# Performance work log

Hardware: AMD Instinct MI355X
Metric: run time of the kernel (lower is better)

## Reference

```python
import jax, jax.numpy as jnp
import numpy as np

N1, N2 = 262144, 65536          # dense / coarse point counts (packed batch)
PREV, SKIP, M0, M1 = 512, 256, 256, 256
EPS_BN = 1e-5                    # torch BatchNorm1d default eps
EPS_DIST = 1e-8


def _bn(x, g, b):
    # BatchNorm1d in training mode: biased batch stats over the point axis
    m = x.mean(axis=0)
    v = x.var(axis=0)
    return (x - m) * jax.lax.rsqrt(v + EPS_BN) * g + b


def setup_inputs() -> dict:
    key = jax.random.key(0)
    ks = jax.random.split(key, 8)
    inp = {
        "points1": jax.random.normal(ks[0], (N1, SKIP), jnp.float32),
        "points2": jax.random.normal(ks[1], (N2, PREV), jnp.float32),
        "dist": jax.random.uniform(ks[2], (N1, 3), jnp.float32),
        "idx": jax.random.randint(ks[3], (N1, 3), 0, N2, dtype=jnp.int32),
        # mlp_f0 / norm_f0
        "Wf0": jax.random.normal(ks[4], (PREV, M0), jnp.float32) / np.sqrt(PREV).astype(np.float32),
        "bf0": jnp.zeros((M0,), jnp.float32),
        "gf0": jnp.ones((M0,), jnp.float32),
        "betaf0": jnp.zeros((M0,), jnp.float32),
        # mlp_s0 / norm_s0 (skip path)
        "Ws0": jax.random.normal(ks[5], (SKIP, M0), jnp.float32) / np.sqrt(SKIP).astype(np.float32),
        "bs0": jnp.zeros((M0,), jnp.float32),
        "gs0": jnp.ones((M0,), jnp.float32),
        "betas0": jnp.zeros((M0,), jnp.float32),
        # mlp_convs[0] / mlp_bns[0]
        "W1": jax.random.normal(ks[6], (M0, M1), jnp.float32) / np.sqrt(M0).astype(np.float32),
        "b1": jnp.zeros((M1,), jnp.float32),
        "g1": jnp.ones((M1,), jnp.float32),
        "beta1": jnp.zeros((M1,), jnp.float32),
    }
    return inp


def reference(points1, points2, dist, idx, Wf0, bf0, gf0, betaf0,
              Ws0, bs0, gs0, betas0, W1, b1, g1, beta1):
    # f0 MLP + BN on coarse features: [N2, PREV] -> [N2, M0]
    p2 = _bn(points2 @ Wf0 + bf0, gf0, betaf0)
    # inverse-distance weights over 3 neighbors: [N1, 3]
    dr = 1.0 / (dist + EPS_DIST)
    w = dr / dr.sum(axis=1, keepdims=True)
    # fused gather + weighted sum: p2[idx] is [N1, 3, M0]
    interp = jnp.einsum('nkc,nk->nc', p2[idx], w)
    # skip path: [N1, SKIP] -> [N1, M0]
    skip = _bn(points1 @ Ws0 + bs0, gs0, betas0)
    x = jax.nn.relu(interp + skip)
    # mlp_convs stack (one layer here): Linear + BN + ReLU
    x = jax.nn.relu(_bn(x @ W1 + b1, g1, beta1))
    return x
```

## Files before the change

### kernel.cpp

```cpp
#include <hip/hip_runtime.h>
#include <hip/hip_bf16.h>

#define CN1 262144
#define CN2 65536
#define CPREV 512
#define CSKIP 256

using u16 = unsigned short;

typedef __attribute__((ext_vector_type(8))) short short8;
typedef __attribute__((ext_vector_type(8))) unsigned short ushort8;
typedef __attribute__((ext_vector_type(4))) float f32x4;
typedef __attribute__((ext_vector_type(8))) float f32x8;

__device__ __forceinline__ float toF(float v) { return v; }
__device__ __forceinline__ float toF(u16 u) { return __uint_as_float(((unsigned)u) << 16); }
__device__ __forceinline__ u16 f2bf(float f) {
    unsigned b = __float_as_uint(f);
    b += 0x7FFFu + ((b >> 16) & 1u);
    return (u16)(b >> 16);
}
__device__ __forceinline__ unsigned pack2(float lo, float hi) {
    return ((unsigned)f2bf(hi) << 16) | (unsigned)f2bf(lo);
}

__global__ __launch_bounds__(256) void transpose_all(
    const float* __restrict__ Wf0, const float* __restrict__ Ws0,
    const float* __restrict__ W1,
    u16* __restrict__ Wtf0, u16* __restrict__ Wts0, u16* __restrict__ Wt1)
{
    int b = blockIdx.x;
    const float* W; u16* Wt; int ksh, e;
    if (b < 512)      { W = Wf0; Wt = Wtf0; ksh = 9; e = b * 256 + threadIdx.x; }
    else if (b < 768) { W = Ws0; Wt = Wts0; ksh = 8; e = (b - 512) * 256 + threadIdx.x; }
    else              { W = W1;  Wt = Wt1;  ksh = 8; e = (b - 768) * 256 + threadIdx.x; }
    int K = 1 << ksh;
    int n = e >> ksh;
    int k = e & (K - 1);
    Wt[e] = f2bf(W[((size_t)k << 8) + n]);
}

template<typename OT>
__device__ __forceinline__ void epilogue(
    f32x4 (&acc)[4][4], u16* AsU, u16* BsU,
    const float* __restrict__ bias, OT* __restrict__ C,
    float* __restrict__ partial, int bm, int t)
{
    const int lane = t & 63;
    const int wid = t >> 6;
    const int wr = wid >> 1;
    const int wrow = wid >> 2;
    const int wcol = wid & 3;
    __syncthreads();
    float* cs  = (float*)AsU;
    float* cs2 = ((float*)AsU) + 512;
    const int r4 = (lane >> 4) * 4;
    const int cc = lane & 15;
    float bv[4];
#pragma unroll
    for (int ni = 0; ni < 4; ++ni) bv[ni] = bias[wcol * 64 + ni * 16 + cc];

#pragma unroll
    for (int ni = 0; ni < 4; ++ni) {
        int col = wcol * 64 + ni * 16 + cc;
        float s = 0.f, s2 = 0.f;
#pragma unroll
        for (int mi = 0; mi < 4; ++mi) {
#pragma unroll
            for (int j = 0; j < 4; ++j) {
                float val = acc[mi][ni][j] + bv[ni];
                s += val;
                s2 = fmaf(val, val, s2);
            }
        }
        s  += __shfl_xor(s, 16);  s  += __shfl_xor(s, 32);
        s2 += __shfl_xor(s2, 16); s2 += __shfl_xor(s2, 32);
        if (lane < 16) { cs[wrow * 256 + col] = s; cs2[wrow * 256 + col] = s2; }
    }

    if constexpr (sizeof(OT) == 2) {
        u16* patchw = BsU + wid * (16 * 72);
        const int trow = lane >> 2;
        const int c16 = (lane & 3) * 16;
#pragma unroll
        for (int mi = 0; mi < 4; ++mi) {
            __syncthreads();
#pragma unroll
            for (int ni = 0; ni < 4; ++ni)
#pragma unroll
                for (int j = 0; j < 4; ++j)
                    patchw[(r4 + j) * 72 + ni * 16 + cc] = f2bf(acc[mi][ni][j] + bv[ni]);
            __syncthreads();
            ushort8 u0 = *(const ushort8*)&patchw[trow * 72 + c16];
            ushort8 u1 = *(const ushort8*)&patchw[trow * 72 + c16 + 8];
            size_t r = (size_t)bm + wrow * 64 + mi * 16 + trow;
            size_t cb = (size_t)wcol * 64 + c16;
            *(ushort8*)((u16*)C + r * 256 + cb) = u0;
            *(ushort8*)((u16*)C + r * 256 + cb + 8) = u1;
        }
    } else {
        float* patchf = ((float*)BsU) + wid * (16 * 36);
        const int trow = lane >> 2;
        const int c8 = (lane & 3) * 8;
#pragma unroll
        for (int mi = 0; mi < 4; ++mi) {
#pragma unroll
            for (int np = 0; np < 2; ++np) {
                __syncthreads();
#pragma unroll
                for (int h = 0; h < 2; ++h) {
                    int ni = np * 2 + h;
#pragma unroll
                    for (int j = 0; j < 4; ++j)
                        patchf[(r4 + j) * 36 + h * 16 + cc] = acc[mi][ni][j] + bv[ni];
                }
                __syncthreads();
                float4 v0 = *(float4*)&patchf[trow * 36 + c8];
                float4 v1 = *(float4*)&patchf[trow * 36 + c8 + 4];
                size_t r = (size_t)bm + wrow * 64 + mi * 16 + trow;
                size_t cb = (size_t)wcol * 64 + np * 32 + c8;
                *(float4*)((float*)C + r * 256 + cb) = v0;
                *(float4*)((float*)C + r * 256 + cb + 4) = v1;
            }
        }
    }
    __syncthreads();
    if (t < 256) {
        partial[(size_t)blockIdx.x * 512 + t]       = cs[t] + cs[256 + t];
        partial[(size_t)blockIdx.x * 512 + 256 + t] = cs2[t] + cs2[256 + t];
    }
    (void)wr;
}

template<int K, typename OT>
__global__ __launch_bounds__(512) void gemm_mfma(
    const float* __restrict__ Af, const u16* __restrict__ Wt,
    const float* __restrict__ bias, OT* __restrict__ C,
    float* __restrict__ partial)
{
    __shared__ u16 As[128 * 40];
    __shared__ u16 Bs[256 * 40];
    const int t = threadIdx.x;
    const int bm = blockIdx.x * 128;
    const int lane = t & 63;
    const int wid = t >> 6;
    const int wrow = wid >> 2;
    const int wcol = wid & 3;

    const int arow = t >> 2;
    const int koff = (t & 3) * 8;

    f32x4 acc[4][4] = {};

    float4 ga0A, ga1A, ga0B, ga1B;
    ushort8 gb0A, gb1A, gb0B, gb1B;

    auto LOADA = [&](int k0) {
        const float* p = Af + (size_t)(bm + arow) * K + k0 + koff;
        ga0A = *(const float4*)p;
        ga1A = *(const float4*)(p + 4);
        const u16* q = Wt + (size_t)arow * K + k0 + koff;
        gb0A = *(const ushort8*)q;
        gb1A = *(const ushort8*)(q + (size_t)128 * K);
    };
    auto LOADB = [&](int k0) {
        const float* p = Af + (size_t)(bm + arow) * K + k0 + koff;
        ga0B = *(const float4*)p;
        ga1B = *(const float4*)(p + 4);
        const u16* q = Wt + (size_t)arow * K + k0 + koff;
        gb0B = *(const ushort8*)q;
        gb1B = *(const ushort8*)(q + (size_t)128 * K);
    };
    auto STAGE = [&](const float4& g0, const float4& g1,
                     const ushort8& b0, const ushort8& b1) {
        uint4 w;
        w.x = pack2(g0.x, g0.y);
        w.y = pack2(g0.z, g0.w);
        w.z = pack2(g1.x, g1.y);
        w.w = pack2(g1.z, g1.w);
        *(uint4*)&As[arow * 40 + koff] = w;
        *(ushort8*)&Bs[arow * 40 + koff] = b0;
        *(ushort8*)&Bs[(128 + arow) * 40 + koff] = b1;
    };
    auto MMA = [&]() {
        const int kq = (lane >> 4) * 8;
        const int rr = lane & 15;
        short8 af[4];
#pragma unroll
        for (int mi = 0; mi < 4; ++mi)
            af[mi] = *(const short8*)&As[(wrow * 64 + mi * 16 + rr) * 40 + kq];
#pragma unroll
        for (int ni = 0; ni < 4; ++ni) {
            short8 bf = *(const short8*)&Bs[(wcol * 64 + ni * 16 + rr) * 40 + kq];
#pragma unroll
            for (int mi = 0; mi < 4; ++mi)
                acc[mi][ni] = __builtin_amdgcn_mfma_f32_16x16x32_bf16(
                    af[mi], bf, acc[mi][ni], 0, 0, 0);
        }
    };

    constexpr int nk = K >> 5;
    LOADA(0);
    LOADB(32);
#pragma unroll
    for (int it = 0; it < nk; it += 2) {
        __syncthreads();
        STAGE(ga0A, ga1A, gb0A, gb1A);
        __syncthreads();
        if (it + 2 < nk) LOADA((it + 2) << 5);
        MMA();
        __syncthreads();
        STAGE(ga0B, ga1B, gb0B, gb1B);
        __syncthreads();
        if (it + 3 < nk) LOADB((it + 3) << 5);
        MMA();
    }

    epilogue<OT>(acc, As, Bs, bias, C, partial, bm, t);
}

template<typename OT>
__global__ __launch_bounds__(512) void gemm_fused(
    const u16* __restrict__ skipb, const u16* __restrict__ y2,
    const float* __restrict__ dist, const int* __restrict__ idx,
    const float* __restrict__ ssf, const float* __restrict__ sss,
    const u16* __restrict__ Wt, const float* __restrict__ bias,
    OT* __restrict__ C, float* __restrict__ partial)
{
    constexpr int K = 256;
    __shared__ u16 As[128 * 40];
    __shared__ u16 Bs[256 * 40];
    __shared__ float sstab[768];
    const int t = threadIdx.x;
    const int bm = blockIdx.x * 128;
    const int lane = t & 63;
    const int wid = t >> 6;
    const int wrow = wid >> 2;
    const int wcol = wid & 3;

    const int arow = t >> 2;
    const int koff = (t & 3) * 8;
    const int row = bm + arow;

    for (int e = t; e < 768; e += 512)
        sstab[e] = (e < 256) ? ssf[e] : sss[e - 256];

    float d0 = dist[row * 3 + 0], d1 = dist[row * 3 + 1], d2 = dist[row * 3 + 2];
    float r0 = 1.f / (d0 + 1e-8f), r1 = 1.f / (d1 + 1e-8f), r2 = 1.f / (d2 + 1e-8f);
    float inv = 1.f / (r0 + r1 + r2);
    const float w0 = r0 * inv, w1 = r1 * inv, w2 = r2 * inv;
    const size_t i0 = (size_t)idx[row * 3 + 0];
    const size_t i1 = (size_t)idx[row * 3 + 1];
    const size_t i2 = (size_t)idx[row * 3 + 2];

    f32x4 acc[4][4] = {};

    ushort8 skA, a0A, a1A, a2A, gb0A, gb1A;
    ushort8 skB, a0B, a1B, a2B, gb0B, gb1B;

    auto LOADA = [&](int k0) {
        const int kc = k0 + koff;
        skA = *(const ushort8*)(skipb + (size_t)row * 256 + kc);
        a0A = *(const ushort8*)(y2 + i0 * 256 + kc);
        a1A = *(const ushort8*)(y2 + i1 * 256 + kc);
        a2A = *(const ushort8*)(y2 + i2 * 256 + kc);
        const u16* q = Wt + (size_t)arow * K + kc;
        gb0A = *(const ushort8*)q;
        gb1A = *(const ushort8*)(q + (size_t)128 * K);
    };
    auto LOADB = [&](int k0) {
        const int kc = k0 + koff;
        skB = *(const ushort8*)(skipb + (size_t)row * 256 + kc);
        a0B = *(const ushort8*)(y2 + i0 * 256 + kc);
        a1B = *(const ushort8*)(y2 + i1 * 256 + kc);
        a2B = *(const ushort8*)(y2 + i2 * 256 + kc);
        const u16* q = Wt + (size_t)arow * K + kc;
        gb0B = *(const ushort8*)q;
        gb1B = *(const ushort8*)(q + (size_t)128 * K);
    };
    auto STAGE = [&](int it, const ushort8& sk8, const ushort8& a0,
                     const ushort8& a1, const ushort8& a2,
                     const ushort8& b0, const ushort8& b1) {
        const int kc = (it << 5) + koff;
        f32x8 sf = *(const f32x8*)&sstab[kc];
        f32x8 sx = *(const f32x8*)&sstab[256 + kc];
        f32x8 ch = *(const f32x8*)&sstab[512 + kc];
        float xs[8];
#pragma unroll
        for (int j = 0; j < 8; ++j) {
            float iv = w0 * toF((u16)a0[j]) + w1 * toF((u16)a1[j])
                     + w2 * toF((u16)a2[j]);
            float val = fmaf(iv, sf[j], fmaf(toF((u16)sk8[j]), sx[j], ch[j]));
            xs[j] = fmaxf(val, 0.f);
        }
        uint4 w;
        w.x = pack2(xs[0], xs[1]);
        w.y = pack2(xs[2], xs[3]);
        w.z = pack2(xs[4], xs[5]);
        w.w = pack2(xs[6], xs[7]);
        *(uint4*)&As[arow * 40 + koff] = w;
        *(ushort8*)&Bs[arow * 40 + koff] = b0;
        *(ushort8*)&Bs[(128 + arow) * 40 + koff] = b1;
    };
    auto MMA = [&]() {
        const int kq = (lane >> 4) * 8;
        const int rr = lane & 15;
        short8 af[4];
#pragma unroll
        for (int mi = 0; mi < 4; ++mi)
            af[mi] = *(const short8*)&As[(wrow * 64 + mi * 16 + rr) * 40 + kq];
#pragma unroll
        for (int ni = 0; ni < 4; ++ni) {
            short8 bf = *(const short8*)&Bs[(wcol * 64 + ni * 16 + rr) * 40 + kq];
#pragma unroll
            for (int mi = 0; mi < 4; ++mi)
                acc[mi][ni] = __builtin_amdgcn_mfma_f32_16x16x32_bf16(
                    af[mi], bf, acc[mi][ni], 0, 0, 0);
        }
    };

    constexpr int nk = K >> 5;
    LOADA(0);
    LOADB(32);
#pragma unroll
    for (int it = 0; it < nk; it += 2) {
        __syncthreads();
        STAGE(it, skA, a0A, a1A, a2A, gb0A, gb1A);
        __syncthreads();
        if (it + 2 < nk) LOADA((it + 2) << 5);
        MMA();
        __syncthreads();
        STAGE(it + 1, skB, a0B, a1B, a2B, gb0B, gb1B);
        __syncthreads();
        if (it + 3 < nk) LOADB((it + 3) << 5);
        MMA();
    }

    epilogue<OT>(acc, As, Bs, bias, C, partial, bm, t);
}

__global__ __launch_bounds__(256) void colstats_final_par(
    const float* __restrict__ partial, int nb, float invR,
    const float* __restrict__ g, const float* __restrict__ beta,
    const float* __restrict__ fold, float* __restrict__ ss)
{
    int c = blockIdx.x;
    int t = threadIdx.x;
    float s = 0.f, s2 = 0.f;
    for (int b = t; b < nb; b += 256) {
        s  += partial[(size_t)b * 512 + c];
        s2 += partial[(size_t)b * 512 + 256 + c];
    }
#pragma unroll
    for (int o = 32; o > 0; o >>= 1) {
        s += __shfl_xor(s, o);
        s2 += __shfl_xor(s2, o);
    }
    __shared__ float rs[4], rs2[4];
    if ((t & 63) == 0) { rs[t >> 6] = s; rs2[t >> 6] = s2; }
    __syncthreads();
    if (t == 0) {
        float S  = rs[0] + rs[1] + rs[2] + rs[3];
        float S2 = rs2[0] + rs2[1] + rs2[2] + rs2[3];
        float m = S * invR;
        float var = fmaf(-m, m, S2 * invR);
        float scale = g[c] * rsqrtf(var + 1e-5f);
        float shift = fmaf(-m, scale, beta[c]);
        if (fold) shift += fold[256 + c];
        ss[c] = scale;
        ss[256 + c] = shift;
    }
}

__global__ __launch_bounds__(256) void bn_relu_cvt(
    const u16* __restrict__ y3, float* __restrict__ out,
    const float* __restrict__ ss)
{
    size_t e = ((size_t)blockIdx.x * 256 + threadIdx.x) * 8;
    int kc = (int)(e & 255);
    ushort8 v = *(const ushort8*)(y3 + e);
    f32x8 sc = *(const f32x8*)(ss + kc);
    f32x8 sh = *(const f32x8*)(ss + 256 + kc);
    float4 o0, o1;
    o0.x = fmaxf(fmaf(toF((u16)v[0]), sc[0], sh[0]), 0.f);
    o0.y = fmaxf(fmaf(toF((u16)v[1]), sc[1], sh[1]), 0.f);
    o0.z = fmaxf(fmaf(toF((u16)v[2]), sc[2], sh[2]), 0.f);
    o0.w = fmaxf(fmaf(toF((u16)v[3]), sc[3], sh[3]), 0.f);
    o1.x = fmaxf(fmaf(toF((u16)v[4]), sc[4], sh[4]), 0.f);
    o1.y = fmaxf(fmaf(toF((u16)v[5]), sc[5], sh[5]), 0.f);
    o1.z = fmaxf(fmaf(toF((u16)v[6]), sc[6], sh[6]), 0.f);
    o1.w = fmaxf(fmaf(toF((u16)v[7]), sc[7], sh[7]), 0.f);
    *(float4*)(out + e) = o0;
    *(float4*)(out + e + 4) = o1;
}

__global__ __launch_bounds__(256) void bn_relu_inplace(
    float* __restrict__ out, const float* __restrict__ ss)
{
    size_t i4 = (size_t)blockIdx.x * 256 + threadIdx.x;
    int c4 = (int)(i4 & 63);
    float4 v = reinterpret_cast<float4*>(out)[i4];
    float4 sc = reinterpret_cast<const float4*>(ss)[c4];
    float4 sh = reinterpret_cast<const float4*>(ss + 256)[c4];
    v.x = fmaxf(fmaf(v.x, sc.x, sh.x), 0.f);
    v.y = fmaxf(fmaf(v.y, sc.y, sh.y), 0.f);
    v.z = fmaxf(fmaf(v.z, sc.z, sh.z), 0.f);
    v.w = fmaxf(fmaf(v.w, sc.w, sh.w), 0.f);
    reinterpret_cast<float4*>(out)[i4] = v;
}

extern "C" void kernel_launch(void* const* d_in, const int* in_sizes, int n_in,
                              void* d_out, int out_size, void* d_ws, size_t ws_size,
                              hipStream_t stream) {
    const float* points1 = (const float*)d_in[0];
    const float* points2 = (const float*)d_in[1];
    const float* dist    = (const float*)d_in[2];
    const int*   idx     = (const int*)d_in[3];
    const float* Wf0     = (const float*)d_in[4];
    const float* bf0     = (const float*)d_in[5];
    const float* gf0     = (const float*)d_in[6];
    const float* betaf0  = (const float*)d_in[7];
    const float* Ws0     = (const float*)d_in[8];
    const float* bs0     = (const float*)d_in[9];
    const float* gs0     = (const float*)d_in[10];
    const float* betas0  = (const float*)d_in[11];
    const float* W1      = (const float*)d_in[12];
    const float* b1      = (const float*)d_in[13];
    const float* g1      = (const float*)d_in[14];
    const float* beta1   = (const float*)d_in[15];

    u16* ws = (u16*)d_ws;
    size_t off = 0;
    u16* y2   = ws + off;  off += (size_t)CN2 * 256;
    u16* xbuf = ws + off;  off += (size_t)CN1 * 256;
    u16* Wtf0 = ws + off;  off += 512 * 256;
    u16* Wts0 = ws + off;  off += 256 * 256;
    u16* Wt1  = ws + off;  off += 256 * 256;
    float* partial = (float*)(ws + off); off += (size_t)2048 * 512 * 2;
    float* ss_f0 = (float*)(ws + off); off += 1024;
    float* ss_s0 = (float*)(ws + off); off += 1024;
    float* ss_1  = (float*)(ws + off); off += 1024;
    u16* y3 = ws + off;
    const size_t NEED = (off + (size_t)CN1 * 256) * 2;
    const bool fused_y3 = (ws_size >= NEED);
    float* out = (float*)d_out;

    transpose_all<<<1024, 256, 0, stream>>>(Wf0, Ws0, W1, Wtf0, Wts0, Wt1);

    gemm_mfma<512, u16><<<CN2 / 128, 512, 0, stream>>>(
        points2, Wtf0, bf0, y2, partial);
    colstats_final_par<<<256, 256, 0, stream>>>(partial, CN2 / 128, 1.0f / CN2,
                                                gf0, betaf0, nullptr, ss_f0);
    gemm_mfma<256, u16><<<CN1 / 128, 512, 0, stream>>>(
        points1, Wts0, bs0, xbuf, partial);
    colstats_final_par<<<256, 256, 0, stream>>>(partial, CN1 / 128, 1.0f / CN1,
                                                gs0, betas0, ss_f0, ss_s0);
    if (fused_y3) {
        gemm_fused<u16><<<CN1 / 128, 512, 0, stream>>>(
            xbuf, y2, dist, idx, ss_f0, ss_s0, Wt1, b1, y3, partial);
    } else {
        gemm_fused<float><<<CN1 / 128, 512, 0, stream>>>(
            xbuf, y2, dist, idx, ss_f0, ss_s0, Wt1, b1, out, partial);
    }
    colstats_final_par<<<256, 256, 0, stream>>>(partial, CN1 / 128, 1.0f / CN1,
                                                g1, beta1, nullptr, ss_1);
    if (fused_y3) {
        bn_relu_cvt<<<32768, 256, 0, stream>>>(y3, out, ss_1);
    } else {
        bn_relu_inplace<<<CN1 / 4, 256, 0, stream>>>(out, ss_1);
    }
}
```

Before: 409.2 us.

## Double-buffer LDS tiles in GEMM kernels to cut barriers per k-step

Both the plain and the fused gather GEMM kernels now use two LDS buffers for the A and B tiles. Each k-step stages the next tile into the idle buffer while MFMA runs on the current one, so there is one barrier per step instead of two. This doubles LDS use per block, which may lower occupancy. The loop is also fully unrolled through a macro.

```diff
diff --git a/kernel.cpp b/kernel.cpp
--- a/kernel.cpp
+++ b/kernel.cpp
@@ -48,7 +48,6 @@
 {
     const int lane = t & 63;
     const int wid = t >> 6;
-    const int wr = wid >> 1;
     const int wrow = wid >> 2;
     const int wcol = wid & 3;
     __syncthreads();
@@ -129,7 +128,6 @@
         partial[(size_t)blockIdx.x * 512 + t]       = cs[t] + cs[256 + t];
         partial[(size_t)blockIdx.x * 512 + 256 + t] = cs2[t] + cs2[256 + t];
     }
-    (void)wr;
 }
 
 template<int K, typename OT>
@@ -138,8 +136,8 @@
     const float* __restrict__ bias, OT* __restrict__ C,
     float* __restrict__ partial)
 {
-    __shared__ u16 As[128 * 40];
-    __shared__ u16 Bs[256 * 40];
+    __shared__ u16 As0[128 * 40], As1[128 * 40];
+    __shared__ u16 Bs0[256 * 40], Bs1[256 * 40];
     const int t = threadIdx.x;
     const int bm = blockIdx.x * 128;
     const int lane = t & 63;
@@ -171,27 +169,27 @@
         gb0B = *(const ushort8*)q;
         gb1B = *(const ushort8*)(q + (size_t)128 * K);
     };
-    auto STAGE = [&](const float4& g0, const float4& g1,
+    auto STAGE = [&](u16* as, u16* bs, const float4& g0, const float4& g1,
                      const ushort8& b0, const ushort8& b1) {
         uint4 w;
         w.x = pack2(g0.x, g0.y);
         w.y = pack2(g0.z, g0.w);
         w.z = pack2(g1.x, g1.y);
         w.w = pack2(g1.z, g1.w);
-        *(uint4*)&As[arow * 40 + koff] = w;
-        *(ushort8*)&Bs[arow * 40 + koff] = b0;
-        *(ushort8*)&Bs[(128 + arow) * 40 + koff] = b1;
-    };
-    auto MMA = [&]() {
+        *(uint4*)&as[arow * 40 + koff] = w;
+        *(ushort8*)&bs[arow * 40 + koff] = b0;
+        *(ushort8*)&bs[(128 + arow) * 40 + koff] = b1;
+    };
+    auto MMA = [&](const u16* as, const u16* bs) {
         const int kq = (lane >> 4) * 8;
         const int rr = lane & 15;
         short8 af[4];
 #pragma unroll
         for (int mi = 0; mi < 4; ++mi)
-            af[mi] = *(const short8*)&As[(wrow * 64 + mi * 16 + rr) * 40 + kq];
+            af[mi] = *(const short8*)&as[(wrow * 64 + mi * 16 + rr) * 40 + kq];
 #pragma unroll
         for (int ni = 0; ni < 4; ++ni) {
-            short8 bf = *(const short8*)&Bs[(wcol * 64 + ni * 16 + rr) * 40 + kq];
+            short8 bf = *(const short8*)&bs[(wcol * 64 + ni * 16 + rr) * 40 + kq];
 #pragma unroll
             for (int mi = 0; mi < 4; ++mi)
                 acc[mi][ni] = __builtin_amdgcn_mfma_f32_16x16x32_bf16(
@@ -202,21 +200,28 @@
     constexpr int nk = K >> 5;
     LOADA(0);
     LOADB(32);
-#pragma unroll
-    for (int it = 0; it < nk; it += 2) {
-        __syncthreads();
-        STAGE(ga0A, ga1A, gb0A, gb1A);
-        __syncthreads();
-        if (it + 2 < nk) LOADA((it + 2) << 5);
-        MMA();
-        __syncthreads();
-        STAGE(ga0B, ga1B, gb0B, gb1B);
-        __syncthreads();
-        if (it + 3 < nk) LOADB((it + 3) << 5);
-        MMA();
-    }
-
-    epilogue<OT>(acc, As, Bs, bias, C, partial, bm, t);
+    STAGE(As0, Bs0, ga0A, ga1A, gb0A, gb1A);
+    __syncthreads();
+
+#define GM_STEP(IT)                                                           \
+    if ((IT) < nk) {                                                          \
+        if ((IT) + 2 < nk) {                                                  \
+            if (((IT)&1) == 0) LOADA(((IT)+2) << 5); else LOADB(((IT)+2) << 5);\
+        }                                                                     \
+        if ((IT) + 1 < nk) {                                                  \
+            if (((IT)&1) == 0) STAGE(As1, Bs1, ga0B, ga1B, gb0B, gb1B);       \
+            else               STAGE(As0, Bs0, ga0A, ga1A, gb0A, gb1A);       \
+        }                                                                     \
+        MMA((((IT)&1) == 0) ? As0 : As1, (((IT)&1) == 0) ? Bs0 : Bs1);        \
+        __syncthreads();                                                      \
+    }
+    GM_STEP(0)  GM_STEP(1)  GM_STEP(2)  GM_STEP(3)
+    GM_STEP(4)  GM_STEP(5)  GM_STEP(6)  GM_STEP(7)
+    GM_STEP(8)  GM_STEP(9)  GM_STEP(10) GM_STEP(11)
+    GM_STEP(12) GM_STEP(13) GM_STEP(14) GM_STEP(15)
+#undef GM_STEP
+
+    epilogue<OT>(acc, As0, Bs0, bias, C, partial, bm, t);
 }
 
 template<typename OT>
@@ -228,8 +233,8 @@
     OT* __restrict__ C, float* __restrict__ partial)
 {
     constexpr int K = 256;
-    __shared__ u16 As[128 * 40];
-    __shared__ u16 Bs[256 * 40];
+    __shared__ u16 As0[128 * 40], As1[128 * 40];
+    __shared__ u16 Bs0[256 * 40], Bs1[256 * 40];
     __shared__ float sstab[768];
     const int t = threadIdx.x;
     const int bm = blockIdx.x * 128;
@@ -278,10 +283,10 @@
         gb0B = *(const ushort8*)q;
         gb1B = *(const ushort8*)(q + (size_t)128 * K);
     };
-    auto STAGE = [&](int it, const ushort8& sk8, const ushort8& a0,
-                     const ushort8& a1, const ushort8& a2,
+    auto STAGE = [&](u16* as, u16* bs, int kstep, const ushort8& sk8,
+                     const ushort8& a0, const ushort8& a1, const ushort8& a2,
                      const ushort8& b0, const ushort8& b1) {
-        const int kc = (it << 5) + koff;
+        const int kc = (kstep << 5) + koff;
         f32x8 sf = *(const f32x8*)&sstab[kc];
         f32x8 sx = *(const f32x8*)&sstab[256 + kc];
         f32x8 ch = *(const f32x8*)&sstab[512 + kc];
@@ -298,20 +303,20 @@
         w.y = pack2(xs[2], xs[3]);
         w.z = pack2(xs[4], xs[5]);
         w.w = pack2(xs[6], xs[7]);
-        *(uint4*)&As[arow * 40 + koff] = w;
-        *(ushort8*)&Bs[arow * 40 + koff] = b0;
-        *(ushort8*)&Bs[(128 + arow) * 40 + koff] = b1;
-    };
-    auto MMA = [&]() {
+        *(uint4*)&as[arow * 40 + koff] = w;
+        *(ushort8*)&bs[arow * 40 + koff] = b0;
+        *(ushort8*)&bs[(128 + arow) * 40 + koff] = b1;
+    };
+    auto MMA = [&](const u16* as, const u16* bs) {
         const int kq = (lane >> 4) * 8;
         const int rr = lane & 15;
         short8 af[4];
 #pragma unroll
         for (int mi = 0; mi < 4; ++mi)
-            af[mi] = *(const short8*)&As[(wrow * 64 + mi * 16 + rr) * 40 + kq];
+            af[mi] = *(const short8*)&as[(wrow * 64 + mi * 16 + rr) * 40 + kq];
 #pragma unroll
         for (int ni = 0; ni < 4; ++ni) {
-            short8 bf = *(const short8*)&Bs[(wcol * 64 + ni * 16 + rr) * 40 + kq];
+            short8 bf = *(const short8*)&bs[(wcol * 64 + ni * 16 + rr) * 40 + kq];
 #pragma unroll
             for (int mi = 0; mi < 4; ++mi)
                 acc[mi][ni] = __builtin_amdgcn_mfma_f32_16x16x32_bf16(
@@ -322,21 +327,29 @@
     constexpr int nk = K >> 5;
     LOADA(0);
     LOADB(32);
-#pragma unroll
-    for (int it = 0; it < nk; it += 2) {
-        __syncthreads();
-        STAGE(it, skA, a0A, a1A, a2A, gb0A, gb1A);
-        __syncthreads();
-        if (it + 2 < nk) LOADA((it + 2) << 5);
-        MMA();
-        __syncthreads();
-        STAGE(it + 1, skB, a0B, a1B, a2B, gb0B, gb1B);
-        __syncthreads();
-        if (it + 3 < nk) LOADB((it + 3) << 5);
-        MMA();
-    }
-
-    epilogue<OT>(acc, As, Bs, bias, C, partial, bm, t);
+    __syncthreads();
+    STAGE(As0, Bs0, 0, skA, a0A, a1A, a2A, gb0A, gb1A);
+    __syncthreads();
+
+#define GF_STEP(IT)                                                           \
+    if ((IT) < nk) {                                                          \
+        if ((IT) + 2 < nk) {                                                  \
+            if (((IT)&1) == 0) LOADA(((IT)+2) << 5); else LOADB(((IT)+2) << 5);\
+        }                                                                     \
+        if ((IT) + 1 < nk) {                                                  \
+            if (((IT)&1) == 0)                                                \
+                STAGE(As1, Bs1, (IT)+1, skB, a0B, a1B, a2B, gb0B, gb1B);      \
+            else                                                              \
+                STAGE(As0, Bs0, (IT)+1, skA, a0A, a1A, a2A, gb0A, gb1A);      \
+        }                                                                     \
+        MMA((((IT)&1) == 0) ? As0 : As1, (((IT)&1) == 0) ? Bs0 : Bs1);        \
+        __syncthreads();                                                      \
+    }
+    GF_STEP(0) GF_STEP(1) GF_STEP(2) GF_STEP(3)
+    GF_STEP(4) GF_STEP(5) GF_STEP(6) GF_STEP(7)
+#undef GF_STEP
+
+    epilogue<OT>(acc, As0, Bs0, bias, C, partial, bm, t);
 }
 
 __global__ __launch_bounds__(256) void colstats_final_par(
```

After: 416.7 us. No clear change (+1.8%).

## Shrink GEMM tiles to 64 rows with 256-thread blocks and single-buffer prefetch

Applied to the files above, without the earlier changes.

All three GEMM kernels go from 128-row tiles with 8 waves to 64-row tiles with 4 waves, and now carry launch bounds that ask for 3 blocks per CU. The double register prefetch (A/B) becomes a single prefetch buffer, and each thread loads a full 32-wide row of B. The aim is higher occupancy and lower register pressure. In exchange, B-tile reuse per block halves, there are twice as many blocks, and the partial-stats buffer and reductions double in size.

```diff
diff --git a/kernel.cpp b/kernel.cpp
--- a/kernel.cpp
+++ b/kernel.cpp
@@ -41,19 +41,16 @@
 }
 
 template<typename OT>
-__device__ __forceinline__ void epilogue(
+__device__ __forceinline__ void epilogue4(
     f32x4 (&acc)[4][4], u16* AsU, u16* BsU,
     const float* __restrict__ bias, OT* __restrict__ C,
     float* __restrict__ partial, int bm, int t)
 {
     const int lane = t & 63;
-    const int wid = t >> 6;
-    const int wr = wid >> 1;
-    const int wrow = wid >> 2;
-    const int wcol = wid & 3;
+    const int wcol = t >> 6;
     __syncthreads();
     float* cs  = (float*)AsU;
-    float* cs2 = ((float*)AsU) + 512;
+    float* cs2 = cs + 256;
     const int r4 = (lane >> 4) * 4;
     const int cc = lane & 15;
     float bv[4];
@@ -75,11 +72,16 @@
         }
         s  += __shfl_xor(s, 16);  s  += __shfl_xor(s, 32);
         s2 += __shfl_xor(s2, 16); s2 += __shfl_xor(s2, 32);
-        if (lane < 16) { cs[wrow * 256 + col] = s; cs2[wrow * 256 + col] = s2; }
+        if (lane < 16) { cs[col] = s; cs2[col] = s2; }
+    }
+    __syncthreads();
+    if (t < 256) {
+        partial[(size_t)blockIdx.x * 512 + t]       = cs[t];
+        partial[(size_t)blockIdx.x * 512 + 256 + t] = cs2[t];
     }
 
     if constexpr (sizeof(OT) == 2) {
-        u16* patchw = BsU + wid * (16 * 72);
+        u16* patchw = BsU + wcol * 1152;
         const int trow = lane >> 2;
         const int c16 = (lane & 3) * 16;
 #pragma unroll
@@ -93,13 +95,13 @@
             __syncthreads();
             ushort8 u0 = *(const ushort8*)&patchw[trow * 72 + c16];
             ushort8 u1 = *(const ushort8*)&patchw[trow * 72 + c16 + 8];
-            size_t r = (size_t)bm + wrow * 64 + mi * 16 + trow;
+            size_t r = (size_t)bm + mi * 16 + trow;
             size_t cb = (size_t)wcol * 64 + c16;
             *(ushort8*)((u16*)C + r * 256 + cb) = u0;
             *(ushort8*)((u16*)C + r * 256 + cb + 8) = u1;
         }
     } else {
-        float* patchf = ((float*)BsU) + wid * (16 * 36);
+        float* patchf = (float*)(BsU + wcol * 1152);
         const int trow = lane >> 2;
         const int c8 = (lane & 3) * 8;
 #pragma unroll
@@ -117,78 +119,66 @@
                 __syncthreads();
                 float4 v0 = *(float4*)&patchf[trow * 36 + c8];
                 float4 v1 = *(float4*)&patchf[trow * 36 + c8 + 4];
-                size_t r = (size_t)bm + wrow * 64 + mi * 16 + trow;
+                size_t r = (size_t)bm + mi * 16 + trow;
                 size_t cb = (size_t)wcol * 64 + np * 32 + c8;
                 *(float4*)((float*)C + r * 256 + cb) = v0;
                 *(float4*)((float*)C + r * 256 + cb + 4) = v1;
             }
         }
     }
-    __syncthreads();
-    if (t < 256) {
-        partial[(size_t)blockIdx.x * 512 + t]       = cs[t] + cs[256 + t];
-        partial[(size_t)blockIdx.x * 512 + 256 + t] = cs2[t] + cs2[256 + t];
-    }
-    (void)wr;
 }
 
 template<int K, typename OT>
-__global__ __launch_bounds__(512) void gemm_mfma(
+__global__ __launch_bounds__(256, 3) void gemm_mfma(
     const float* __restrict__ Af, const u16* __restrict__ Wt,
     const float* __restrict__ bias, OT* __restrict__ C,
     float* __restrict__ partial)
 {
-    __shared__ u16 As[128 * 40];
+    __shared__ u16 As[64 * 40];
     __shared__ u16 Bs[256 * 40];
     const int t = threadIdx.x;
-    const int bm = blockIdx.x * 128;
+    const int bm = blockIdx.x * 64;
     const int lane = t & 63;
-    const int wid = t >> 6;
-    const int wrow = wid >> 2;
-    const int wcol = wid & 3;
+    const int wcol = t >> 6;
 
     const int arow = t >> 2;
     const int koff = (t & 3) * 8;
+    const int brow = t;
+    const int rr = lane & 15;
+    const int kq = (lane >> 4) * 8;
 
     f32x4 acc[4][4] = {};
 
-    float4 ga0A, ga1A, ga0B, ga1B;
-    ushort8 gb0A, gb1A, gb0B, gb1B;
-
-    auto LOADA = [&](int k0) {
+    float4 ga0, ga1;
+    ushort8 gb0, gb1, gb2, gb3;
+
+    auto LOAD = [&](int k0) {
         const float* p = Af + (size_t)(bm + arow) * K + k0 + koff;
-        ga0A = *(const float4*)p;
-        ga1A = *(const float4*)(p + 4);
-        const u16* q = Wt + (size_t)arow * K + k0 + koff;
-        gb0A = *(const ushort8*)q;
-        gb1A = *(const ushort8*)(q + (size_t)128 * K);
-    };
-    auto LOADB = [&](int k0) {
-        const float* p = Af + (size_t)(bm + arow) * K + k0 + koff;
-        ga0B = *(const float4*)p;
-        ga1B = *(const float4*)(p + 4);
-        const u16* q = Wt + (size_t)arow * K + k0 + koff;
-        gb0B = *(const ushort8*)q;
-        gb1B = *(const ushort8*)(q + (size_t)128 * K);
-    };
-    auto STAGE = [&](const float4& g0, const float4& g1,
-                     const ushort8& b0, const ushort8& b1) {
+        ga0 = *(const float4*)p;
+        ga1 = *(const float4*)(p + 4);
+        const u16* q = Wt + (size_t)brow * K + k0;
+        gb0 = *(const ushort8*)q;
+        gb1 = *(const ushort8*)(q + 8);
+        gb2 = *(const ushort8*)(q + 16);
+        gb3 = *(const ushort8*)(q + 24);
+    };
+    auto STAGE = [&]() {
         uint4 w;
-        w.x = pack2(g0.x, g0.y);
-        w.y = pack2(g0.z, g0.w);
-        w.z = pack2(g1.x, g1.y);
-        w.w = pack2(g1.z, g1.w);
+        w.x = pack2(ga0.x, ga0.y);
+        w.y = pack2(ga0.z, ga0.w);
+        w.z = pack2(ga1.x, ga1.y);
+        w.w = pack2(ga1.z, ga1.w);
         *(uint4*)&As[arow * 40 + koff] = w;
-        *(ushort8*)&Bs[arow * 40 + koff] = b0;
-        *(ushort8*)&Bs[(128 + arow) * 40 + koff] = b1;
+        *(ushort8*)&Bs[brow * 40]      = gb0;
+        *(ushort8*)&Bs[brow * 40 + 8]  = gb1;
+        *(ushort8*)&Bs[brow * 40 + 16] = gb2;
+        *(ushort8*)&Bs[brow * 40 + 24] = gb3;
     };
     auto MMA = [&]() {
-        const int kq = (lane >> 4) * 8;
-        const int rr = lane & 15;
         short8 af[4];
 #pragma unroll
         for (int mi = 0; mi < 4; ++mi)
-            af[mi] = *(const short8*)&As[(wrow * 64 + mi * 16 + rr) * 40 + kq];
+            af[mi] = *(const short8*)&As[(mi * 16 + rr) * 40 + kq];
 #pragma unroll
         for (int ni = 0; ni < 4; ++ni) {
             short8 bf = *(const short8*)&Bs[(wcol * 64 + ni * 16 + rr) * 40 + kq];
@@ -200,27 +190,20 @@
     };
 
     constexpr int nk = K >> 5;
-    LOADA(0);
-    LOADB(32);
-#pragma unroll
-    for (int it = 0; it < nk; it += 2) {
+    LOAD(0);
+    for (int it = 0; it < nk; ++it) {
         __syncthreads();
-        STAGE(ga0A, ga1A, gb0A, gb1A);
+        STAGE();
         __syncthreads();
-        if (it + 2 < nk) LOADA((it + 2) << 5);
+        if (it + 1 < nk) LOAD((it + 1) << 5);
         MMA();
-        __syncthreads();
-        STAGE(ga0B, ga1B, gb0B, gb1B);
-        __syncthreads();
-        if (it + 3 < nk) LOADB((it + 3) << 5);
-        MMA();
-    }
-
-    epilogue<OT>(acc, As, Bs, bias, C, partial, bm, t);
+    }
+
+    epilogue4<OT>(acc, As, Bs, bias, C, partial, bm, t);
 }
 
 template<typename OT>
-__global__ __launch_bounds__(512) void gemm_fused(
+__global__ __launch_bounds__(256, 3) void gemm_fused(
     const u16* __restrict__ skipb, const u16* __restrict__ y2,
     const float* __restrict__ dist, const int* __restrict__ idx,
     const float* __restrict__ ssf, const float* __restrict__ sss,
@@ -228,60 +211,52 @@
     OT* __restrict__ C, float* __restrict__ partial)
 {
     constexpr int K = 256;
-    __shared__ u16 As[128 * 40];
+    __shared__ u16 As[64 * 40];
     __shared__ u16 Bs[256 * 40];
     __shared__ float sstab[768];
     const int t = threadIdx.x;
-    const int bm = blockIdx.x * 128;
+    const int bm = blockIdx.x * 64;
     const int lane = t & 63;
-    const int wid = t >> 6;
-    const int wrow = wid >> 2;
-    const int wcol = wid & 3;
+    const int wcol = t >> 6;
 
     const int arow = t >> 2;
     const int koff = (t & 3) * 8;
+    const int brow = t;
+    const int rr = lane & 15;
+    const int kq = (lane >> 4) * 8;
     const int row = bm + arow;
 
-    for (int e = t; e < 768; e += 512)
+    for (int e = t; e < 768; e += 256)
         sstab[e] = (e < 256) ? ssf[e] : sss[e - 256];
 
     float d0 = dist[row * 3 + 0], d1 = dist[row * 3 + 1], d2 = dist[row * 3 + 2];
     float r0 = 1.f / (d0 + 1e-8f), r1 = 1.f / (d1 + 1e-8f), r2 = 1.f / (d2 + 1e-8f);
     float inv = 1.f / (r0 + r1 + r2);
     const float w0 = r0 * inv, w1 = r1 * inv, w2 = r2 * inv;
-    const size_t i0 = (size_t)idx[row * 3 + 0];
-    const size_t i1 = (size_t)idx[row * 3 + 1];
-    const size_t i2 = (size_t)idx[row * 3 + 2];
+    const unsigned i0 = (unsigned)idx[row * 3 + 0];
+    const unsigned i1 = (unsigned)idx[row * 3 + 1];
+    const unsigned i2 = (unsigned)idx[row * 3 + 2];
 
     f32x4 acc[4][4] = {};
 
-    ushort8 skA, a0A, a1A, a2A, gb0A, gb1A;
-    ushort8 skB, a0B, a1B, a2B, gb0B, gb1B;
-
-    auto LOADA = [&](int k0) {
+    ushort8 sk8, a0, a1, a2;
+    ushort8 gb0, gb1, gb2, gb3;
+    int kcur = 0;
+
+    auto LOAD = [&](int k0) {
         const int kc = k0 + koff;
-        skA = *(const ushort8*)(skipb + (size_t)row * 256 + kc);
-        a0A = *(const ushort8*)(y2 + i0 * 256 + kc);
-        a1A = *(const ushort8*)(y2 + i1 * 256 + kc);
-        a2A = *(const ushort8*)(y2 + i2 * 256 + kc);
-        const u16* q = Wt + (size_t)arow * K + kc;
-        gb0A = *(const ushort8*)q;
-        gb1A = *(const ushort8*)(q + (size_t)128 * K);
-    };
-    auto LOADB = [&](int k0) {
-        const int kc = k0 + koff;
-        skB = *(const ushort8*)(skipb + (size_t)row * 256 + kc);
-        a0B = *(const ushort8*)(y2 + i0 * 256 + kc);
-        a1B = *(const ushort8*)(y2 + i1 * 256 + kc);
-        a2B = *(const ushort8*)(y2 + i2 * 256 + kc);
-        const u16* q = Wt + (size_t)arow * K + kc;
-        gb0B = *(const ushort8*)q;
-        gb1B = *(const ushort8*)(q + (size_t)128 * K);
-    };
-    auto STAGE = [&](int it, const ushort8& sk8, const ushort8& a0,
-                     const ushort8& a1, const ushort8& a2,
-                     const ushort8& b0, const ushort8& b1) {
-        const int kc = (it << 5) + koff;
+        sk8 = *(const ushort8*)(skipb + (size_t)row * 256 + kc);
+        a0  = *(const ushort8*)(y2 + (size_t)i0 * 256 + kc);
+        a1  = *(const ushort8*)(y2 + (size_t)i1 * 256 + kc);
+        a2  = *(const ushort8*)(y2 + (size_t)i2 * 256 + kc);
+        const u16* q = Wt + (size_t)brow * K + k0;
+        gb0 = *(const ushort8*)q;
+        gb1 = *(const ushort8*)(q + 8);
+        gb2 = *(const ushort8*)(q + 16);
+        gb3 = *(const ushort8*)(q + 24);
+    };
+    auto STAGE = [&]() {
+        const int kc = kcur + koff;
         f32x8 sf = *(const f32x8*)&sstab[kc];
         f32x8 sx = *(const f32x8*)&sstab[256 + kc];
         f32x8 ch = *(const f32x8*)&sstab[512 + kc];
@@ -299,16 +274,16 @@
         w.z = pack2(xs[4], xs[5]);
         w.w = pack2(xs[6], xs[7]);
         *(uint4*)&As[arow * 40 + koff] = w;
-        *(ushort8*)&Bs[arow * 40 + koff] = b0;
-        *(ushort8*)&Bs[(128 + arow) * 40 + koff] = b1;
+        *(ushort8*)&Bs[brow * 40]      = gb0;
+        *(ushort8*)&Bs[brow * 40 + 8]  = gb1;
+        *(ushort8*)&Bs[brow * 40 + 16] = gb2;
+        *(ushort8*)&Bs[brow * 40 + 24] = gb3;
     };
     auto MMA = [&]() {
-        const int kq = (lane >> 4) * 8;
-        const int rr = lane & 15;
         short8 af[4];
 #pragma unroll
         for (int mi = 0; mi < 4; ++mi)
-            af[mi] = *(const short8*)&As[(wrow * 64 + mi * 16 + rr) * 40 + kq];
+            af[mi] = *(const short8*)&As[(mi * 16 + rr) * 40 + kq];
 #pragma unroll
         for (int ni = 0; ni < 4; ++ni) {
             short8 bf = *(const short8*)&Bs[(wcol * 64 + ni * 16 + rr) * 40 + kq];
@@ -320,23 +295,16 @@
     };
 
     constexpr int nk = K >> 5;
-    LOADA(0);
-    LOADB(32);
-#pragma unroll
-    for (int it = 0; it < nk; it += 2) {
+    LOAD(0);
+    for (int it = 0; it < nk; ++it) {
         __syncthreads();
-        STAGE(it, skA, a0A, a1A, a2A, gb0A, gb1A);
+        STAGE();
         __syncthreads();
-        if (it + 2 < nk) LOADA((it + 2) << 5);
+        if (it + 1 < nk) { kcur = (it + 1) << 5; LOAD(kcur); }
         MMA();
-        __syncthreads();
-        STAGE(it + 1, skB, a0B, a1B, a2B, gb0B, gb1B);
-        __syncthreads();
-        if (it + 3 < nk) LOADB((it + 3) << 5);
-        MMA();
-    }
-
-    epilogue<OT>(acc, As, Bs, bias, C, partial, bm, t);
+    }
+
+    epilogue4<OT>(acc, As, Bs, bias, C, partial, bm, t);
 }
 
 __global__ __launch_bounds__(256) void colstats_final_par(
@@ -436,7 +404,7 @@
     u16* Wtf0 = ws + off;  off += 512 * 256;
     u16* Wts0 = ws + off;  off += 256 * 256;
     u16* Wt1  = ws + off;  off += 256 * 256;
-    float* partial = (float*)(ws + off); off += (size_t)2048 * 512 * 2;
+    float* partial = (float*)(ws + off); off += (size_t)4096 * 512 * 2;
     float* ss_f0 = (float*)(ws + off); off += 1024;
     float* ss_s0 = (float*)(ws + off); off += 1024;
     float* ss_1  = (float*)(ws + off); off += 1024;
@@ -447,22 +415,22 @@
 
     transpose_all<<<1024, 256, 0, stream>>>(Wf0, Ws0, W1, Wtf0, Wts0, Wt1);
 
-    gemm_mfma<512, u16><<<CN2 / 128, 512, 0, stream>>>(
+    gemm_mfma<512, u16><<<CN2 / 64, 256, 0, stream>>>(
         points2, Wtf0, bf0, y2, partial);
-    colstats_final_par<<<256, 256, 0, stream>>>(partial, CN2 / 128, 1.0f / CN2,
+    colstats_final_par<<<256, 256, 0, stream>>>(partial, CN2 / 64, 1.0f / CN2,
                                                 gf0, betaf0, nullptr, ss_f0);
-    gemm_mfma<256, u16><<<CN1 / 128, 512, 0, stream>>>(
+    gemm_mfma<256, u16><<<CN1 / 64, 256, 0, stream>>>(
         points1, Wts0, bs0, xbuf, partial);
-    colstats_final_par<<<256, 256, 0, stream>>>(partial, CN1 / 128, 1.0f / CN1,
+    colstats_final_par<<<256, 256, 0, stream>>>(partial, CN1 / 64, 1.0f / CN1,
                                                 gs0, betas0, ss_f0, ss_s0);
     if (fused_y3) {
-        gemm_fused<u16><<<CN1 / 128, 512, 0, stream>>>(
+        gemm_fused<u16><<<CN1 / 64, 256, 0, stream>>>(
             xbuf, y2, dist, idx, ss_f0, ss_s0, Wt1, b1, y3, partial);
     } else {
-        gemm_fused<float><<<CN1 / 128, 512, 0, stream>>>(
+        gemm_fused<float><<<CN1 / 64, 256, 0, stream>>>(
             xbuf, y2, dist, idx, ss_f0, ss_s0, Wt1, b1, out, partial);
     }
-    colstats_final_par<<<256, 256, 0, stream>>>(partial, CN1 / 128, 1.0f / CN1,
+    colstats_final_par<<<256, 256, 0, stream>>>(partial, CN1 / 64, 1.0f / CN1,
                                                 g1, beta1, nullptr, ss_1);
     if (fused_y3) {
         bn_relu_cvt<<<32768, 256, 0, stream>>>(y3, out, ss_1);
```

New measurement: 504.7 us. +23.3%, slower.

## Stage full 256-wide A panel in LDS once, stream only B tiles

Applied to the files above, without the earlier changes.

The GEMM kernels now load and convert a whole 128x256 slab of the A operand into a larger padded LDS buffer up front, including the gather, interpolation and skip fusion in the second GEMM. The K-loop then streams only 32-wide weight tiles through a single register buffer. This removes the per-step A staging and the double-buffered register sets, and lets all gather loads for a row be issued together. In exchange, LDS use per block rises to about 66 KB, which may lower occupancy, and A loads are no longer overlapped with the MFMA work.

```diff
diff --git a/kernel.cpp b/kernel.cpp
--- a/kernel.cpp
+++ b/kernel.cpp
@@ -41,19 +41,18 @@
 }
 
 template<typename OT>
-__device__ __forceinline__ void epilogue(
-    f32x4 (&acc)[4][4], u16* AsU, u16* BsU,
+__device__ __forceinline__ void epilogue8(
+    f32x4 (&acc)[4][4], u16* Ax, u16* Bs,
     const float* __restrict__ bias, OT* __restrict__ C,
     float* __restrict__ partial, int bm, int t)
 {
     const int lane = t & 63;
     const int wid = t >> 6;
-    const int wr = wid >> 1;
     const int wrow = wid >> 2;
     const int wcol = wid & 3;
     __syncthreads();
-    float* cs  = (float*)AsU;
-    float* cs2 = ((float*)AsU) + 512;
+    float* cs  = (float*)Ax;
+    float* cs2 = ((float*)Ax) + 512;
     const int r4 = (lane >> 4) * 4;
     const int cc = lane & 15;
     float bv[4];
@@ -79,7 +78,7 @@
     }
 
     if constexpr (sizeof(OT) == 2) {
-        u16* patchw = BsU + wid * (16 * 72);
+        u16* patchw = Bs + wid * 1152;
         const int trow = lane >> 2;
         const int c16 = (lane & 3) * 16;
 #pragma unroll
@@ -99,7 +98,7 @@
             *(ushort8*)((u16*)C + r * 256 + cb + 8) = u1;
         }
     } else {
-        float* patchf = ((float*)BsU) + wid * (16 * 36);
+        float* patchf = (float*)(Bs + wid * 1152);
         const int trow = lane >> 2;
         const int c8 = (lane & 3) * 8;
 #pragma unroll
@@ -129,7 +128,6 @@
         partial[(size_t)blockIdx.x * 512 + t]       = cs[t] + cs[256 + t];
         partial[(size_t)blockIdx.x * 512 + 256 + t] = cs2[t] + cs2[256 + t];
     }
-    (void)wr;
 }
 
 template<int K, typename OT>
@@ -138,7 +136,7 @@
     const float* __restrict__ bias, OT* __restrict__ C,
     float* __restrict__ partial)
 {
-    __shared__ u16 As[128 * 40];
+    __shared__ u16 Ax[128 * 264];
     __shared__ u16 Bs[256 * 40];
     const int t = threadIdx.x;
     const int bm = blockIdx.x * 128;
@@ -148,47 +146,29 @@
     const int wcol = wid & 3;
 
     const int arow = t >> 2;
-    const int koff = (t & 3) * 8;
+    const int q4 = t & 3;
+    const int brow = t >> 1;
+    const int bko = (t & 1) * 16;
+    const int rr = lane & 15;
+    const int kq = (lane >> 4) * 8;
 
     f32x4 acc[4][4] = {};
-
-    float4 ga0A, ga1A, ga0B, ga1B;
-    ushort8 gb0A, gb1A, gb0B, gb1B;
-
-    auto LOADA = [&](int k0) {
-        const float* p = Af + (size_t)(bm + arow) * K + k0 + koff;
-        ga0A = *(const float4*)p;
-        ga1A = *(const float4*)(p + 4);
-        const u16* q = Wt + (size_t)arow * K + k0 + koff;
-        gb0A = *(const ushort8*)q;
-        gb1A = *(const ushort8*)(q + (size_t)128 * K);
-    };
+    ushort8 gb0, gb1;
+
     auto LOADB = [&](int k0) {
-        const float* p = Af + (size_t)(bm + arow) * K + k0 + koff;
-        ga0B = *(const float4*)p;
-        ga1B = *(const float4*)(p + 4);
-        const u16* q = Wt + (size_t)arow * K + k0 + koff;
-        gb0B = *(const ushort8*)q;
-        gb1B = *(const ushort8*)(q + (size_t)128 * K);
-    };
-    auto STAGE = [&](const float4& g0, const float4& g1,
-                     const ushort8& b0, const ushort8& b1) {
-        uint4 w;
-        w.x = pack2(g0.x, g0.y);
-        w.y = pack2(g0.z, g0.w);
-        w.z = pack2(g1.x, g1.y);
-        w.w = pack2(g1.z, g1.w);
-        *(uint4*)&As[arow * 40 + koff] = w;
-        *(ushort8*)&Bs[arow * 40 + koff] = b0;
-        *(ushort8*)&Bs[(128 + arow) * 40 + koff] = b1;
-    };
-    auto MMA = [&]() {
-        const int kq = (lane >> 4) * 8;
-        const int rr = lane & 15;
+        const u16* q = Wt + (size_t)brow * K + k0 + bko;
+        gb0 = *(const ushort8*)q;
+        gb1 = *(const ushort8*)(q + 8);
+    };
+    auto STAGEB = [&]() {
+        *(ushort8*)&Bs[brow * 40 + bko] = gb0;
+        *(ushort8*)&Bs[brow * 40 + bko + 8] = gb1;
+    };
+    auto MMA = [&](int it) {
         short8 af[4];
 #pragma unroll
         for (int mi = 0; mi < 4; ++mi)
-            af[mi] = *(const short8*)&As[(wrow * 64 + mi * 16 + rr) * 40 + kq];
+            af[mi] = *(const short8*)&Ax[(wrow * 64 + mi * 16 + rr) * 264 + it * 32 + kq];
 #pragma unroll
         for (int ni = 0; ni < 4; ++ni) {
             short8 bf = *(const short8*)&Bs[(wcol * 64 + ni * 16 + rr) * 40 + kq];
@@ -199,24 +179,32 @@
         }
     };
 
-    constexpr int nk = K >> 5;
-    LOADA(0);
-    LOADB(32);
-#pragma unroll
-    for (int it = 0; it < nk; it += 2) {
+#pragma unroll
+    for (int h = 0; h < K / 256; ++h) {
         __syncthreads();
-        STAGE(ga0A, ga1A, gb0A, gb1A);
-        __syncthreads();
-        if (it + 2 < nk) LOADA((it + 2) << 5);
-        MMA();
-        __syncthreads();
-        STAGE(ga0B, ga1B, gb0B, gb1B);
-        __syncthreads();
-        if (it + 3 < nk) LOADB((it + 3) << 5);
-        MMA();
-    }
-
-    epilogue<OT>(acc, As, Bs, bias, C, partial, bm, t);
+        {
+            const float* base = Af + (size_t)(bm + arow) * K + h * 256 + q4 * 64;
+#pragma unroll
+            for (int c = 0; c < 8; ++c) {
+                float4 f0 = *(const float4*)(base + c * 8);
+                float4 f1 = *(const float4*)(base + c * 8 + 4);
+                uint4 w;
+                w.x = pack2(f0.x, f0.y); w.y = pack2(f0.z, f0.w);
+                w.z = pack2(f1.x, f1.y); w.w = pack2(f1.z, f1.w);
+                *(uint4*)&Ax[arow * 264 + q4 * 64 + c * 8] = w;
+            }
+        }
+        LOADB(h * 256);
+        for (int it = 0; it < 8; ++it) {
+            __syncthreads();
+            STAGEB();
+            __syncthreads();
+            if (it + 1 < 8) LOADB(h * 256 + (it + 1) * 32);
+            MMA(it);
+        }
+    }
+
+    epilogue8<OT>(acc, Ax, Bs, bias, C, partial, bm, t);
 }
 
 template<typename OT>
@@ -228,7 +216,7 @@
     OT* __restrict__ C, float* __restrict__ partial)
 {
     constexpr int K = 256;
-    __shared__ u16 As[128 * 40];
+    __shared__ u16 Ax[128 * 264];
     __shared__ u16 Bs[256 * 40];
     __shared__ float sstab[768];
     const int t = threadIdx.x;
@@ -239,7 +227,11 @@
     const int wcol = wid & 3;
 
     const int arow = t >> 2;
-    const int koff = (t & 3) * 8;
+    const int q4 = t & 3;
+    const int brow = t >> 1;
+    const int bko = (t & 1) * 16;
+    const int rr = lane & 15;
+    const int kq = (lane >> 4) * 8;
     const int row = bm + arow;
 
     for (int e = t; e < 768; e += 512)
@@ -249,66 +241,27 @@
     float r0 = 1.f / (d0 + 1e-8f), r1 = 1.f / (d1 + 1e-8f), r2 = 1.f / (d2 + 1e-8f);
     float inv = 1.f / (r0 + r1 + r2);
     const float w0 = r0 * inv, w1 = r1 * inv, w2 = r2 * inv;
-    const size_t i0 = (size_t)idx[row * 3 + 0];
-    const size_t i1 = (size_t)idx[row * 3 + 1];
-    const size_t i2 = (size_t)idx[row * 3 + 2];
+    const unsigned i0 = (unsigned)idx[row * 3 + 0];
+    const unsigned i1 = (unsigned)idx[row * 3 + 1];
+    const unsigned i2 = (unsigned)idx[row * 3 + 2];
 
     f32x4 acc[4][4] = {};
-
-    ushort8 skA, a0A, a1A, a2A, gb0A, gb1A;
-    ushort8 skB, a0B, a1B, a2B, gb0B, gb1B;
-
-    auto LOADA = [&](int k0) {
-        const int kc = k0 + koff;
-        skA = *(const ushort8*)(skipb + (size_t)row * 256 + kc);
-        a0A = *(const ushort8*)(y2 + i0 * 256 + kc);
-        a1A = *(const ushort8*)(y2 + i1 * 256 + kc);
-        a2A = *(const ushort8*)(y2 + i2 * 256 + kc);
-        const u16* q = Wt + (size_t)arow * K + kc;
-        gb0A = *(const ushort8*)q;
-        gb1A = *(const ushort8*)(q + (size_t)128 * K);
-    };
+    ushort8 gb0, gb1;
+
     auto LOADB = [&](int k0) {
-        const int kc = k0 + koff;
-        skB = *(const ushort8*)(skipb + (size_t)row * 256 + kc);
-        a0B = *(const ushort8*)(y2 + i0 * 256 + kc);
-        a1B = *(const ushort8*)(y2 + i1 * 256 + kc);
-        a2B = *(const ushort8*)(y2 + i2 * 256 + kc);
-        const u16* q = Wt + (size_t)arow * K + kc;
-        gb0B = *(const ushort8*)q;
-        gb1B = *(const ushort8*)(q + (size_t)128 * K);
-    };
-    auto STAGE = [&](int it, const ushort8& sk8, const ushort8& a0,
-                     const ushort8& a1, const ushort8& a2,
-                     const ushort8& b0, const ushort8& b1) {
-        const int kc = (it << 5) + koff;
-        f32x8 sf = *(const f32x8*)&sstab[kc];
-        f32x8 sx = *(const f32x8*)&sstab[256 + kc];
-        f32x8 ch = *(const f32x8*)&sstab[512 + kc];
-        float xs[8];
-#pragma unroll
-        for (int j = 0; j < 8; ++j) {
-            float iv = w0 * toF((u16)a0[j]) + w1 * toF((u16)a1[j])
-                     + w2 * toF((u16)a2[j]);
-            float val = fmaf(iv, sf[j], fmaf(toF((u16)sk8[j]), sx[j], ch[j]));
-            xs[j] = fmaxf(val, 0.f);
-        }
-        uint4 w;
-        w.x = pack2(xs[0], xs[1]);
-        w.y = pack2(xs[2], xs[3]);
-        w.z = pack2(xs[4], xs[5]);
-        w.w = pack2(xs[6], xs[7]);
-        *(uint4*)&As[arow * 40 + koff] = w;
-        *(ushort8*)&Bs[arow * 40 + koff] = b0;
-        *(ushort8*)&Bs[(128 + arow) * 40 + koff] = b1;
-    };
-    auto MMA = [&]() {
-        const int kq = (lane >> 4) * 8;
-        const int rr = lane & 15;
+        const u16* q = Wt + (size_t)brow * K + k0 + bko;
+        gb0 = *(const ushort8*)q;
+        gb1 = *(const ushort8*)(q + 8);
+    };
+    auto STAGEB = [&]() {
+        *(ushort8*)&Bs[brow * 40 + bko] = gb0;
+        *(ushort8*)&Bs[brow * 40 + bko + 8] = gb1;
+    };
+    auto MMA = [&](int it) {
         short8 af[4];
 #pragma unroll
         for (int mi = 0; mi < 4; ++mi)
-            af[mi] = *(const short8*)&As[(wrow * 64 + mi * 16 + rr) * 40 + kq];
+            af[mi] = *(const short8*)&Ax[(wrow * 64 + mi * 16 + rr) * 264 + it * 32 + kq];
 #pragma unroll
         for (int ni = 0; ni < 4; ++ni) {
             short8 bf = *(const short8*)&Bs[(wcol * 64 + ni * 16 + rr) * 40 + kq];
@@ -319,24 +272,44 @@
         }
     };
 
-    constexpr int nk = K >> 5;
-    LOADA(0);
-    LOADB(32);
-#pragma unroll
-    for (int it = 0; it < nk; it += 2) {
+    __syncthreads();
+    {
+#pragma unroll
+        for (int c = 0; c < 8; ++c) {
+            const int kc = q4 * 64 + c * 8;
+            ushort8 sk = *(const ushort8*)(skipb + (size_t)row * 256 + kc);
+            ushort8 a0 = *(const ushort8*)(y2 + (size_t)i0 * 256 + kc);
+            ushort8 a1 = *(const ushort8*)(y2 + (size_t)i1 * 256 + kc);
+            ushort8 a2 = *(const ushort8*)(y2 + (size_t)i2 * 256 + kc);
+            f32x8 sf = *(const f32x8*)&sstab[kc];
+            f32x8 sx = *(const f32x8*)&sstab[256 + kc];
+            f32x8 ch = *(const f32x8*)&sstab[512 + kc];
+            float xs[8];
+#pragma unroll
+            for (int j = 0; j < 8; ++j) {
+                float iv = w0 * toF((u16)a0[j]) + w1 * toF((u16)a1[j])
+                         + w2 * toF((u16)a2[j]);
+                float val = fmaf(iv, sf[j], fmaf(toF((u16)sk[j]), sx[j], ch[j]));
+                xs[j] = fmaxf(val, 0.f);
+            }
+            uint4 w;
+            w.x = pack2(xs[0], xs[1]);
+            w.y = pack2(xs[2], xs[3]);
+            w.z = pack2(xs[4], xs[5]);
+            w.w = pack2(xs[6], xs[7]);
+            *(uint4*)&Ax[arow * 264 + kc] = w;
+        }
+    }
+    LOADB(0);
+    for (int it = 0; it < 8; ++it) {
         __syncthreads();
-        STAGE(it, skA, a0A, a1A, a2A, gb0A, gb1A);
+        STAGEB();
         __syncthreads();
-        if (it + 2 < nk) LOADA((it + 2) << 5);
-        MMA();
-        __syncthreads();
-        STAGE(it + 1, skB, a0B, a1B, a2B, gb0B, gb1B);
-        __syncthreads();
-        if (it + 3 < nk) LOADB((it + 3) << 5);
-        MMA();
-    }
-
-    epilogue<OT>(acc, As, Bs, bias, C, partial, bm, t);
+        if (it + 1 < 8) LOADB((it + 1) * 32);
+        MMA(it);
+    }
+
+    epilogue8<OT>(acc, Ax, Bs, bias, C, partial, bm, t);
 }
 
 __global__ __launch_bounds__(256) void colstats_final_par(
```

New measurement: 782.8 us. +91.3%, slower.
